# Kernel tuning notes

Measured on AMD Instinct MI355X. Metric: run time of the kernel, lower is better.

Reference implementation:

```python
import jax, jax.numpy as jnp
import numpy as np

H, L, D, R = 16, 4096, 64, 128   # heads, seq len, head dim, FAVOR+ feature dim
S_SCALE = 0.125                  # attention inner-product scaling S
CHUNK = 128                      # chunk size for causal linear attention
EPS = 1e-10                      # module's self.epsilon denominator guard


def _get_proj(d, r, seed=0):
    # get_proj(R, D, orthogonal=True, hyperbolic=True): QR-orthogonalized
    # Gaussian block rescaled by chi column norms, then [W, -W].
    rng = np.random.RandomState(seed)
    rh = r // 2
    w = rng.randn(d, rh)
    chis = np.linalg.norm(w, ord=2, axis=0, keepdims=True)
    qm, _ = np.linalg.qr(w, mode='reduced')
    w = qm * chis
    return np.concatenate((w, -w), axis=1).astype(np.float32)  # (D, R)


def setup_inputs() -> dict:
    key = jax.random.key(0)
    kq, kk, kv = jax.random.split(key, 3)
    q = jax.random.normal(kq, (H, L, D), dtype=jnp.float32)
    k = jax.random.normal(kk, (H, L, D), dtype=jnp.float32)
    v = jax.random.normal(kv, (H, L, D), dtype=jnp.float32)
    W = jnp.asarray(_get_proj(D, R))
    return {"T": 64, "k": k, "q": q, "v": v, "W": W}


def _phi(x, W):
    # FAVOR+ feature map: x' = x * S^0.5 / D^0.25;
    # phi(x) = exp(W^T x' - ||x'||^2 / 2) / sqrt(R)
    xs = x * (S_SCALE ** 0.5 / D ** 0.25)            # (H, L, D)
    Wx = jnp.einsum('hld,dr->hlr', xs, W)            # (H, L, R)
    sq = 0.5 * jnp.sum(xs * xs, axis=-1, keepdims=True)
    return jnp.exp(Wx - sq) / (R ** 0.5)             # (H, L, R)


def reference(T, k, q, v, W):
    # Deterministic FAVOR+ estimator of the strictly-causal softmax attention
    # Pred_l = sum_{j<l} v_j exp(S<q_l,k_j>) / sum_{i<l} exp(S<q_l,k_i>)
    # which the tree+sampling machinery approximates (T = sampling budget,
    # irrelevant for the exact kernel estimate). Chunked linear attention.
    del T
    pq = _phi(q, W)                                  # (H, L, R)
    pk = _phi(k, W)                                  # (H, L, R)
    nc = L // CHUNK
    pq_c = pq.reshape(H, nc, CHUNK, R)
    pk_c = pk.reshape(H, nc, CHUNK, R)
    v_c = v.reshape(H, nc, CHUNK, D)
    # per-chunk KV summaries and exclusive prefix over chunks
    skv = jnp.einsum('hncr,hncd->hnrd', pk_c, v_c)   # (H, nc, R, D)
    zk = jnp.sum(pk_c, axis=2)                       # (H, nc, R)
    skv_prev = jnp.cumsum(skv, axis=1) - skv         # exclusive
    zk_prev = jnp.cumsum(zk, axis=1) - zk
    num_inter = jnp.einsum('hncr,hnrd->hncd', pq_c, skv_prev)
    den_inter = jnp.einsum('hncr,hnr->hnc', pq_c, zk_prev)
    # intra-chunk strictly-causal part (j < l)
    A = jnp.einsum('hncr,hnsr->hncs', pq_c, pk_c)    # (H, nc, C, C)
    mask = jnp.tril(jnp.ones((CHUNK, CHUNK), dtype=A.dtype), k=-1)
    A = A * mask
    num_intra = jnp.einsum('hncs,hnsd->hncd', A, v_c)
    den_intra = jnp.sum(A, axis=-1)
    out = (num_inter + num_intra) / (den_inter + den_intra + EPS)[..., None]
    return out.reshape(H, L, D)
```

## Files before the change

### kernel.cpp

```cpp
#include <hip/hip_runtime.h>
#include <hip/hip_bf16.h>

#define H 16
#define L 4096
#define D 64
#define R 128
#define C2 64
#define NC2 64
#define HN2 (H * NC2)
#define EPS 1e-10f
#define XS_SCALE 0.125f
#define PHI_SCALE 0.08838834764831845f

typedef __attribute__((ext_vector_type(8))) short bf8;
typedef __attribute__((ext_vector_type(4))) short bf4;
typedef __attribute__((ext_vector_type(16))) float facc16;

static __device__ __forceinline__ unsigned short f2b(float f) {
    union { __hip_bfloat16 h; unsigned short u; } c;
    c.h = __float2bfloat16(f);
    return c.u;
}
static __device__ __forceinline__ float b2f(unsigned short s) {
    return __uint_as_float(((unsigned)s) << 16);
}

__global__ __launch_bounds__(256) void kW(const float* __restrict__ W,
                                          unsigned short* __restrict__ WF) {
    __shared__ float wl[8192];
    for (int i = threadIdx.x; i < 8192; i += 256) wl[i] = W[i];
    __syncthreads();
    for (int i = threadIdx.x; i < 1024; i += 256) {
        int tile = i >> 8, s = (i >> 6) & 3, hi = (i >> 5) & 1, lo = i & 31;
        int r = tile * 32 + lo;
        #pragma unroll
        for (int e = 0; e < 8; ++e)
            WF[i * 8 + e] = f2b(wl[(16 * s + 8 * hi + e) * 128 + r]);
    }
}

__global__ __launch_bounds__(256, 4) void k1(
    const float* __restrict__ q, const float* __restrict__ k,
    const float* __restrict__ v, const unsigned short* __restrict__ WF,
    unsigned short* __restrict__ pqF, unsigned short* __restrict__ pkF,
    unsigned short* __restrict__ vTF, unsigned short* __restrict__ skvTp,
    float* __restrict__ zk)
{
    __shared__ __align__(16) unsigned short A_[8192];
    __shared__ __align__(16) unsigned short C_[8192];
    const int tid = threadIdx.x, hn = blockIdx.x;
    const int lane = tid & 63, wave = tid >> 6, lo = lane & 31, hi = lane >> 5;
    const int rg = wave & 1, ch = wave >> 1;
    const size_t cbase = (size_t)hn * C2 * D;

    bf8 af[4];
    float sqrow[16];
    {
        float ssq = 0.f;
        #pragma unroll
        for (int s = 0; s < 4; ++s) {
            const float* qp = q + cbase + (rg * 32 + lo) * 64 + 16 * s + 8 * hi;
            float4 f0 = *(const float4*)qp;
            float4 f1 = *(const float4*)(qp + 4);
            float x0 = f0.x * XS_SCALE, x1 = f0.y * XS_SCALE, x2 = f0.z * XS_SCALE, x3 = f0.w * XS_SCALE;
            float x4 = f1.x * XS_SCALE, x5 = f1.y * XS_SCALE, x6 = f1.z * XS_SCALE, x7 = f1.w * XS_SCALE;
            ssq += x0*x0 + x1*x1 + x2*x2 + x3*x3 + x4*x4 + x5*x5 + x6*x6 + x7*x7;
            bf8 a;
            a[0]=(short)f2b(x0); a[1]=(short)f2b(x1); a[2]=(short)f2b(x2); a[3]=(short)f2b(x3);
            a[4]=(short)f2b(x4); a[5]=(short)f2b(x5); a[6]=(short)f2b(x6); a[7]=(short)f2b(x7);
            af[s] = a;
        }
        ssq += __shfl_xor(ssq, 32); ssq *= 0.5f;
        #pragma unroll
        for (int r2 = 0; r2 < 16; ++r2)
            sqrow[r2] = __shfl(ssq, (r2 & 3) + 8 * (r2 >> 2) + 4 * hi);
    }
    {
        facc16 acc[2];
        #pragma unroll
        for (int t = 0; t < 2; ++t)
            #pragma unroll
            for (int e = 0; e < 16; ++e) acc[t][e] = 0.f;
        #pragma unroll
        for (int s = 0; s < 4; ++s)
            #pragma unroll
            for (int t = 0; t < 2; ++t) {
                const bf8 b = *(const bf8*)(WF + (((2 * ch + t) * 4 + s) * 64 + hi * 32 + lo) * 8);
                acc[t] = __builtin_amdgcn_mfma_f32_32x32x16_bf16(af[s], b, acc[t], 0, 0, 0);
            }
        #pragma unroll
        for (int t = 0; t < 2; ++t)
            #pragma unroll
            for (int reg = 0; reg < 16; ++reg) {
                int row = rg * 32 + (reg & 3) + 8 * (reg >> 2) + 4 * hi;
                int col = (2 * ch + t) * 32 + lo;
                C_[(unsigned)((row * 128 + col) ^ ((row & 15) << 3))] =
                    f2b(__expf(acc[t][reg] - sqrow[reg]) * PHI_SCALE);
            }
    }
    __syncthreads();

    {
        int g2 = wave & 1, sh = wave >> 1;
        #pragma unroll
        for (int s2 = 0; s2 < 4; ++s2) {
            int s = sh * 4 + s2;
            bf8 t8 = *(const bf8*)&C_[(unsigned)(((g2 * 32 + lo) * 128 + 16 * s + 8 * hi) ^ ((lo & 15) << 3))];
            *(bf8*)(pqF + (size_t)hn * 8192 + (size_t)(((g2 * 8 + s) * 64 + hi * 32 + lo) * 8)) = t8;
        }
    }
    float sqk[16];
    {
        float ssq = 0.f;
        #pragma unroll
        for (int s = 0; s < 4; ++s) {
            const float* kp = k + cbase + (rg * 32 + lo) * 64 + 16 * s + 8 * hi;
            float4 f0 = *(const float4*)kp;
            float4 f1 = *(const float4*)(kp + 4);
            float x0 = f0.x * XS_SCALE, x1 = f0.y * XS_SCALE, x2 = f0.z * XS_SCALE, x3 = f0.w * XS_SCALE;
            float x4 = f1.x * XS_SCALE, x5 = f1.y * XS_SCALE, x6 = f1.z * XS_SCALE, x7 = f1.w * XS_SCALE;
            ssq += x0*x0 + x1*x1 + x2*x2 + x3*x3 + x4*x4 + x5*x5 + x6*x6 + x7*x7;
            bf8 a;
            a[0]=(short)f2b(x0); a[1]=(short)f2b(x1); a[2]=(short)f2b(x2); a[3]=(short)f2b(x3);
            a[4]=(short)f2b(x4); a[5]=(short)f2b(x5); a[6]=(short)f2b(x6); a[7]=(short)f2b(x7);
            af[s] = a;
        }
        ssq += __shfl_xor(ssq, 32); ssq *= 0.5f;
        #pragma unroll
        for (int r2 = 0; r2 < 16; ++r2)
            sqk[r2] = __shfl(ssq, (r2 & 3) + 8 * (r2 >> 2) + 4 * hi);
    }
    facc16 acck[2];
    #pragma unroll
    for (int t = 0; t < 2; ++t)
        #pragma unroll
        for (int e = 0; e < 16; ++e) acck[t][e] = 0.f;
    #pragma unroll
    for (int s = 0; s < 4; ++s)
        #pragma unroll
        for (int t = 0; t < 2; ++t) {
            const bf8 b = *(const bf8*)(WF + (((2 * ch + t) * 4 + s) * 64 + hi * 32 + lo) * 8);
            acck[t] = __builtin_amdgcn_mfma_f32_32x32x16_bf16(af[s], b, acck[t], 0, 0, 0);
        }
    __syncthreads();

    #pragma unroll
    for (int t = 0; t < 2; ++t) {
        int colr = (2 * ch + t) * 32 + lo;
        #pragma unroll
        for (int g = 0; g < 4; ++g) {
            int c0 = rg * 32 + 8 * g + 4 * hi;
            bf4 pk4;
            #pragma unroll
            for (int e = 0; e < 4; ++e) {
                unsigned short bb = f2b(__expf(acck[t][4 * g + e] - sqk[4 * g + e]) * PHI_SCALE);
                pk4[e] = (short)bb;
                C_[(unsigned)(((c0 + e) * 128 + colr) ^ (((c0 + e) & 15) << 3))] = bb;
            }
            *(bf4*)&A_[(unsigned)((colr * 64 + c0) ^ ((colr & 7) << 3))] = pk4;
        }
    }
    __syncthreads();

    {
        int g2 = wave & 1, sh = wave >> 1;
        #pragma unroll
        for (int s2 = 0; s2 < 4; ++s2) {
            int s = sh * 4 + s2;
            bf8 t8 = *(const bf8*)&C_[(unsigned)(((g2 * 32 + lo) * 128 + 16 * s + 8 * hi) ^ ((lo & 15) << 3))];
            *(bf8*)(pkF + (size_t)hn * 8192 + (size_t)(((g2 * 8 + s) * 64 + hi * 32 + lo) * 8)) = t8;
        }
    }
    {
        bf8 onesk;
        #pragma unroll
        for (int e = 0; e < 8; ++e) onesk[e] = (lo == 0) ? (short)0x3F80 : (short)0;
        facc16 az;
        #pragma unroll
        for (int e = 0; e < 16; ++e) az[e] = 0.f;
        #pragma unroll
        for (int s = 0; s < 4; ++s) {
            const bf8 a = *(const bf8*)&A_[(unsigned)(((wave * 32 + lo) * 64 + 16 * s + 8 * hi) ^ ((lo & 7) << 3))];
            az = __builtin_amdgcn_mfma_f32_32x32x16_bf16(a, onesk, az, 0, 0, 0);
        }
        if (lo == 0) {
            #pragma unroll
            for (int reg = 0; reg < 16; ++reg)
                zk[(size_t)hn * 128 + wave * 32 + (reg & 3) + 8 * (reg >> 2) + 4 * hi] = az[reg];
        }
    }
    facc16 tv;
    {
        bf8 aid[2];
        #pragma unroll
        for (int s2 = 0; s2 < 2; ++s2)
            #pragma unroll
            for (int e = 0; e < 8; ++e)
                aid[s2][e] = (e == lo - 16 * s2 - 8 * hi) ? (short)0x3F80 : (short)0;
        #pragma unroll
        for (int e = 0; e < 16; ++e) tv[e] = 0.f;
        #pragma unroll
        for (int s2 = 0; s2 < 2; ++s2) {
            const float* vp = v + cbase + (size_t)(32 * rg + lo) * 64 + 16 * (2 * ch + s2) + 8 * hi;
            float4 f0 = *(const float4*)vp;
            float4 f1 = *(const float4*)(vp + 4);
            bf8 b;
            b[0]=(short)f2b(f0.x); b[1]=(short)f2b(f0.y); b[2]=(short)f2b(f0.z); b[3]=(short)f2b(f0.w);
            b[4]=(short)f2b(f1.x); b[5]=(short)f2b(f1.y); b[6]=(short)f2b(f1.z); b[7]=(short)f2b(f1.w);
            tv = __builtin_amdgcn_mfma_f32_32x32x16_bf16(aid[s2], b, tv, 0, 0, 0);
        }
    }
    __syncthreads();

    #pragma unroll
    for (int reg = 0; reg < 16; ++reg) {
        int d = 32 * ch + (reg & 3) + 8 * (reg >> 2) + 4 * hi;
        int c = 32 * rg + lo;
        C_[(unsigned)((d * 64 + c) ^ ((d & 7) << 3))] = f2b(tv[reg]);
    }
    __syncthreads();

    {
        int g2 = wave & 1, sh = wave >> 1;
        #pragma unroll
        for (int s2 = 0; s2 < 2; ++s2) {
            int s = sh * 2 + s2;
            bf8 t8 = *(const bf8*)&C_[(unsigned)(((g2 * 32 + lo) * 64 + 16 * s + 8 * hi) ^ ((lo & 7) << 3))];
            *(bf8*)(vTF + (size_t)hn * 4096 + (size_t)(((g2 * 4 + s) * 64 + hi * 32 + lo) * 8)) = t8;
        }
    }
    {
        facc16 acs[2];
        #pragma unroll
        for (int t = 0; t < 2; ++t)
            #pragma unroll
            for (int e = 0; e < 16; ++e) acs[t][e] = 0.f;
        #pragma unroll
        for (int s = 0; s < 4; ++s) {
            const bf8 a = *(const bf8*)&C_[(unsigned)(((rg * 32 + lo) * 64 + 16 * s + 8 * hi) ^ ((lo & 7) << 3))];
            #pragma unroll
            for (int t = 0; t < 2; ++t) {
                const bf8 b = *(const bf8*)&A_[(unsigned)((((2 * ch + t) * 32 + lo) * 64 + 16 * s + 8 * hi) ^ ((lo & 7) << 3))];
                acs[t] = __builtin_amdgcn_mfma_f32_32x32x16_bf16(a, b, acs[t], 0, 0, 0);
            }
        }
        unsigned short* sg = skvTp + (size_t)hn * 8192;
        #pragma unroll
        for (int t = 0; t < 2; ++t)
            #pragma unroll
            for (int reg = 0; reg < 16; ++reg) {
                int d = rg * 32 + (reg & 3) + 8 * (reg >> 2) + 4 * hi;
                int r = (2 * ch + t) * 32 + lo;
                sg[d * 128 + r] = f2b(acs[t][reg]);
            }
    }
}

__global__ __launch_bounds__(256) void k2(unsigned short* __restrict__ skvTp,
                                          const float* __restrict__ zk,
                                          unsigned short* __restrict__ zkp)
{
    const int bid = blockIdx.x, tid = threadIdx.x;
    if (bid < 512) {
        int g = bid * 256 + tid;
        int h = g >> 13, dr = g & 8191;
        unsigned short* p = skvTp + (size_t)h * NC2 * 8192 + dr;
        unsigned short vals[NC2];
        #pragma unroll
        for (int n = 0; n < NC2; ++n) vals[n] = p[(size_t)n * 8192];
        float run = 0.f;
        #pragma unroll
        for (int n = 0; n < NC2; ++n) {
            float t = b2f(vals[n]);
            p[(size_t)n * 8192] = f2b(run);
            run += t;
        }
    } else {
        int g2 = (bid - 512) * 256 + tid;
        int h = g2 >> 7, r = g2 & 127;
        const float* pz = zk + (size_t)h * NC2 * 128 + r;
        unsigned short* oz = zkp + (size_t)h * NC2 * 128 + r;
        float vals[NC2];
        #pragma unroll
        for (int n = 0; n < NC2; ++n) vals[n] = pz[n * 128];
        float run = 0.f;
        #pragma unroll
        for (int n = 0; n < NC2; ++n) {
            oz[n * 128] = f2b(run);
            run += vals[n];
        }
    }
}

__global__ __launch_bounds__(256) void k3(
    const unsigned short* __restrict__ pqF, const unsigned short* __restrict__ pkF,
    const unsigned short* __restrict__ vTF, const unsigned short* __restrict__ skvTp,
    const unsigned short* __restrict__ zkp, float* __restrict__ out)
{
    __shared__ __align__(16) unsigned short S_[4096];
    const int tid = threadIdx.x, hn = blockIdx.x;
    const int lane = tid & 63, wave = tid >> 6, lo = lane & 31, hi = lane >> 5;
    const int rg = wave & 1, ch = wave >> 1;

    bf8 qf[8];
    #pragma unroll
    for (int s = 0; s < 8; ++s)
        qf[s] = *(const bf8*)(pqF + (size_t)hn * 8192 + (size_t)(((rg * 8 + s) * 64 + hi * 32 + lo) * 8));
    bf8 onesf, zf[8];
    #pragma unroll
    for (int e = 0; e < 8; ++e) onesf[e] = (lo == 0) ? (short)0x3F80 : (short)0;
    #pragma unroll
    for (int s = 0; s < 8; ++s)
        #pragma unroll
        for (int e = 0; e < 8; ++e) zf[s][e] = 0;
    if (lo == 0) {
        #pragma unroll
        for (int s = 0; s < 8; ++s)
            zf[s] = *(const bf8*)(zkp + (size_t)hn * 128 + 16 * s + 8 * hi);
    }

    facc16 ac1;
    #pragma unroll
    for (int e = 0; e < 16; ++e) ac1[e] = 0.f;
    #pragma unroll
    for (int s = 0; s < 8; ++s) {
        const bf8 b = *(const bf8*)(pkF + (size_t)hn * 8192 + (size_t)(((ch * 8 + s) * 64 + hi * 32 + lo) * 8));
        ac1 = __builtin_amdgcn_mfma_f32_32x32x16_bf16(qf[s], b, ac1, 0, 0, 0);
    }
    #pragma unroll
    for (int reg = 0; reg < 16; ++reg) {
        int row = rg * 32 + (reg & 3) + 8 * (reg >> 2) + 4 * hi;
        int sc = ch * 32 + lo;
        S_[(unsigned)((row * 64 + sc) ^ ((row & 7) << 3))] = f2b(sc < row ? ac1[reg] : 0.f);
    }
    __syncthreads();

    facc16 an, ad;
    #pragma unroll
    for (int e = 0; e < 16; ++e) { an[e] = 0.f; ad[e] = 0.f; }
    #pragma unroll
    for (int s = 0; s < 4; ++s) {
        const bf8 a = *(const bf8*)&S_[(unsigned)(((rg * 32 + lo) * 64 + 16 * s + 8 * hi) ^ ((lo & 7) << 3))];
        const bf8 b = *(const bf8*)(vTF + (size_t)hn * 4096 + (size_t)(((ch * 4 + s) * 64 + hi * 32 + lo) * 8));
        an = __builtin_amdgcn_mfma_f32_32x32x16_bf16(a, b, an, 0, 0, 0);
        ad = __builtin_amdgcn_mfma_f32_32x32x16_bf16(a, onesf, ad, 0, 0, 0);
    }
    #pragma unroll
    for (int s = 0; s < 8; ++s) {
        const bf8 b = *(const bf8*)(skvTp + (size_t)hn * 8192 + (size_t)(ch * 32 + lo) * 128 + 16 * s + 8 * hi);
        an = __builtin_amdgcn_mfma_f32_32x32x16_bf16(qf[s], b, an, 0, 0, 0);
        ad = __builtin_amdgcn_mfma_f32_32x32x16_bf16(qf[s], zf[s], ad, 0, 0, 0);
    }
    float* og = out + (size_t)hn * C2 * D;
    #pragma unroll
    for (int reg = 0; reg < 16; ++reg) {
        int row = rg * 32 + (reg & 3) + 8 * (reg >> 2) + 4 * hi;
        float dv = __shfl(ad[reg], lane & 32);
        og[row * 64 + ch * 32 + lo] = an[reg] / (dv + EPS);
    }
}

extern "C" void kernel_launch(void* const* d_in, const int* in_sizes, int n_in,
                              void* d_out, int out_size, void* d_ws, size_t ws_size,
                              hipStream_t stream) {
    const float* k = (const float*)d_in[1];
    const float* q = (const float*)d_in[2];
    const float* v = (const float*)d_in[3];
    const float* W = (const float*)d_in[4];
    float* out = (float*)d_out;

    unsigned short* pqF   = (unsigned short*)d_ws;
    unsigned short* pkF   = pqF + (size_t)HN2 * 8192;
    unsigned short* vTF   = pkF + (size_t)HN2 * 8192;
    unsigned short* skvTp = vTF + (size_t)HN2 * 4096;
    unsigned short* WF    = skvTp + (size_t)HN2 * 8192;
    unsigned short* zkp   = WF + 8192;
    float* zk             = (float*)(zkp + (size_t)HN2 * 128);

    kW<<<1, 256, 0, stream>>>(W, WF);
    k1<<<HN2, 256, 0, stream>>>(q, k, v, WF, pqF, pkF, vTF, skvTp, zk);
    k2<<<520, 256, 0, stream>>>(skvTp, zk, zkp);
    k3<<<HN2, 256, 0, stream>>>(pqF, pkF, vTF, skvTp, zkp, out);
}
```

Before: 54.48 us.

## Compute phi(q) inside k3 instead of storing it from k1

Moves the q feature-map computation (projection, exp) out of k1 and into k3, where phi(q) is written to shared memory and read directly as MFMA operands. This removes the global write and re-read of the bf16 pqF buffer and shortens k1. In exchange k3 reads fp32 q and WF, uses more LDS (an extra 16 KB), and adds a barrier. k1's LDS layout also changes, with V getting its own buffer, which removes one barrier there.

```diff
diff --git a/kernel.cpp b/kernel.cpp
--- a/kernel.cpp
+++ b/kernel.cpp
@@ -40,22 +40,217 @@
 }
 
 __global__ __launch_bounds__(256, 4) void k1(
-    const float* __restrict__ q, const float* __restrict__ k,
-    const float* __restrict__ v, const unsigned short* __restrict__ WF,
-    unsigned short* __restrict__ pqF, unsigned short* __restrict__ pkF,
-    unsigned short* __restrict__ vTF, unsigned short* __restrict__ skvTp,
-    float* __restrict__ zk)
+    const float* __restrict__ k, const float* __restrict__ v,
+    const unsigned short* __restrict__ WF,
+    unsigned short* __restrict__ pkF, unsigned short* __restrict__ vTF,
+    unsigned short* __restrict__ skvTp, float* __restrict__ zk)
 {
+    __shared__ __align__(16) unsigned short C_[8192];
     __shared__ __align__(16) unsigned short A_[8192];
-    __shared__ __align__(16) unsigned short C_[8192];
+    __shared__ __align__(16) unsigned short V_[4096];
     const int tid = threadIdx.x, hn = blockIdx.x;
     const int lane = tid & 63, wave = tid >> 6, lo = lane & 31, hi = lane >> 5;
     const int rg = wave & 1, ch = wave >> 1;
     const size_t cbase = (size_t)hn * C2 * D;
 
     bf8 af[4];
-    float sqrow[16];
-    {
+    float sqk[16];
+    {
+        float ssq = 0.f;
+        #pragma unroll
+        for (int s = 0; s < 4; ++s) {
+            const float* kp = k + cbase + (rg * 32 + lo) * 64 + 16 * s + 8 * hi;
+            float4 f0 = *(const float4*)kp;
+            float4 f1 = *(const float4*)(kp + 4);
+            float x0 = f0.x * XS_SCALE, x1 = f0.y * XS_SCALE, x2 = f0.z * XS_SCALE, x3 = f0.w * XS_SCALE;
+            float x4 = f1.x * XS_SCALE, x5 = f1.y * XS_SCALE, x6 = f1.z * XS_SCALE, x7 = f1.w * XS_SCALE;
+            ssq += x0*x0 + x1*x1 + x2*x2 + x3*x3 + x4*x4 + x5*x5 + x6*x6 + x7*x7;
+            bf8 a;
+            a[0]=(short)f2b(x0); a[1]=(short)f2b(x1); a[2]=(short)f2b(x2); a[3]=(short)f2b(x3);
+            a[4]=(short)f2b(x4); a[5]=(short)f2b(x5); a[6]=(short)f2b(x6); a[7]=(short)f2b(x7);
+            af[s] = a;
+        }
+        ssq += __shfl_xor(ssq, 32); ssq *= 0.5f;
+        #pragma unroll
+        for (int r2 = 0; r2 < 16; ++r2)
+            sqk[r2] = __shfl(ssq, (r2 & 3) + 8 * (r2 >> 2) + 4 * hi);
+    }
+    {
+        facc16 acck[2];
+        #pragma unroll
+        for (int t = 0; t < 2; ++t)
+            #pragma unroll
+            for (int e = 0; e < 16; ++e) acck[t][e] = 0.f;
+        #pragma unroll
+        for (int s = 0; s < 4; ++s)
+            #pragma unroll
+            for (int t = 0; t < 2; ++t) {
+                const bf8 b = *(const bf8*)(WF + (((2 * ch + t) * 4 + s) * 64 + hi * 32 + lo) * 8);
+                acck[t] = __builtin_amdgcn_mfma_f32_32x32x16_bf16(af[s], b, acck[t], 0, 0, 0);
+            }
+        #pragma unroll
+        for (int t = 0; t < 2; ++t) {
+            int colr = (2 * ch + t) * 32 + lo;
+            #pragma unroll
+            for (int g = 0; g < 4; ++g) {
+                int c0 = rg * 32 + 8 * g + 4 * hi;
+                bf4 pk4;
+                #pragma unroll
+                for (int e = 0; e < 4; ++e) {
+                    unsigned short bb = f2b(__expf(acck[t][4 * g + e] - sqk[4 * g + e]) * PHI_SCALE);
+                    pk4[e] = (short)bb;
+                    C_[(unsigned)(((c0 + e) * 128 + colr) ^ (((c0 + e) & 15) << 3))] = bb;
+                }
+                *(bf4*)&A_[(unsigned)((colr * 64 + c0) ^ ((colr & 7) << 3))] = pk4;
+            }
+        }
+    }
+    __syncthreads();
+
+    {
+        int g2 = wave & 1, sh = wave >> 1;
+        #pragma unroll
+        for (int s2 = 0; s2 < 4; ++s2) {
+            int s = sh * 4 + s2;
+            bf8 t8 = *(const bf8*)&C_[(unsigned)(((g2 * 32 + lo) * 128 + 16 * s + 8 * hi) ^ ((lo & 15) << 3))];
+            *(bf8*)(pkF + (size_t)hn * 8192 + (size_t)(((g2 * 8 + s) * 64 + hi * 32 + lo) * 8)) = t8;
+        }
+    }
+    {
+        bf8 onesk;
+        #pragma unroll
+        for (int e = 0; e < 8; ++e) onesk[e] = (lo == 0) ? (short)0x3F80 : (short)0;
+        facc16 az;
+        #pragma unroll
+        for (int e = 0; e < 16; ++e) az[e] = 0.f;
+        #pragma unroll
+        for (int s = 0; s < 4; ++s) {
+            const bf8 a = *(const bf8*)&A_[(unsigned)(((wave * 32 + lo) * 64 + 16 * s + 8 * hi) ^ ((lo & 7) << 3))];
+            az = __builtin_amdgcn_mfma_f32_32x32x16_bf16(a, onesk, az, 0, 0, 0);
+        }
+        if (lo == 0) {
+            #pragma unroll
+            for (int reg = 0; reg < 16; ++reg)
+                zk[(size_t)hn * 128 + wave * 32 + (reg & 3) + 8 * (reg >> 2) + 4 * hi] = az[reg];
+        }
+    }
+    {
+        bf8 aid[2];
+        #pragma unroll
+        for (int s2 = 0; s2 < 2; ++s2)
+            #pragma unroll
+            for (int e = 0; e < 8; ++e)
+                aid[s2][e] = (e == lo - 16 * s2 - 8 * hi) ? (short)0x3F80 : (short)0;
+        facc16 tv;
+        #pragma unroll
+        for (int e = 0; e < 16; ++e) tv[e] = 0.f;
+        #pragma unroll
+        for (int s2 = 0; s2 < 2; ++s2) {
+            const float* vp = v + cbase + (size_t)(32 * rg + lo) * 64 + 16 * (2 * ch + s2) + 8 * hi;
+            float4 f0 = *(const float4*)vp;
+            float4 f1 = *(const float4*)(vp + 4);
+            bf8 b;
+            b[0]=(short)f2b(f0.x); b[1]=(short)f2b(f0.y); b[2]=(short)f2b(f0.z); b[3]=(short)f2b(f0.w);
+            b[4]=(short)f2b(f1.x); b[5]=(short)f2b(f1.y); b[6]=(short)f2b(f1.z); b[7]=(short)f2b(f1.w);
+            tv = __builtin_amdgcn_mfma_f32_32x32x16_bf16(aid[s2], b, tv, 0, 0, 0);
+        }
+        #pragma unroll
+        for (int reg = 0; reg < 16; ++reg) {
+            int d = 32 * ch + (reg & 3) + 8 * (reg >> 2) + 4 * hi;
+            int c = 32 * rg + lo;
+            V_[(unsigned)((d * 64 + c) ^ ((d & 7) << 3))] = f2b(tv[reg]);
+        }
+    }
+    __syncthreads();
+
+    {
+        int g2 = wave & 1, sh = wave >> 1;
+        #pragma unroll
+        for (int s2 = 0; s2 < 2; ++s2) {
+            int s = sh * 2 + s2;
+            bf8 t8 = *(const bf8*)&V_[(unsigned)(((g2 * 32 + lo) * 64 + 16 * s + 8 * hi) ^ ((lo & 7) << 3))];
+            *(bf8*)(vTF + (size_t)hn * 4096 + (size_t)(((g2 * 4 + s) * 64 + hi * 32 + lo) * 8)) = t8;
+        }
+    }
+    {
+        facc16 acs[2];
+        #pragma unroll
+        for (int t = 0; t < 2; ++t)
+            #pragma unroll
+            for (int e = 0; e < 16; ++e) acs[t][e] = 0.f;
+        #pragma unroll
+        for (int s = 0; s < 4; ++s) {
+            const bf8 a = *(const bf8*)&V_[(unsigned)(((rg * 32 + lo) * 64 + 16 * s + 8 * hi) ^ ((lo & 7) << 3))];
+            #pragma unroll
+            for (int t = 0; t < 2; ++t) {
+                const bf8 b = *(const bf8*)&A_[(unsigned)((((2 * ch + t) * 32 + lo) * 64 + 16 * s + 8 * hi) ^ ((lo & 7) << 3))];
+                acs[t] = __builtin_amdgcn_mfma_f32_32x32x16_bf16(a, b, acs[t], 0, 0, 0);
+            }
+        }
+        unsigned short* sg = skvTp + (size_t)hn * 8192;
+        #pragma unroll
+        for (int t = 0; t < 2; ++t)
+            #pragma unroll
+            for (int reg = 0; reg < 16; ++reg) {
+                int d = rg * 32 + (reg & 3) + 8 * (reg >> 2) + 4 * hi;
+                int r = (2 * ch + t) * 32 + lo;
+                sg[d * 128 + r] = f2b(acs[t][reg]);
+            }
+    }
+}
+
+__global__ __launch_bounds__(256) void k2(unsigned short* __restrict__ skvTp,
+                                          const float* __restrict__ zk,
+                                          unsigned short* __restrict__ zkp)
+{
+    const int bid = blockIdx.x, tid = threadIdx.x;
+    if (bid < 512) {
+        int g = bid * 256 + tid;
+        int h = g >> 13, dr = g & 8191;
+        unsigned short* p = skvTp + (size_t)h * NC2 * 8192 + dr;
+        unsigned short vals[NC2];
+        #pragma unroll
+        for (int n = 0; n < NC2; ++n) vals[n] = p[(size_t)n * 8192];
+        float run = 0.f;
+        #pragma unroll
+        for (int n = 0; n < NC2; ++n) {
+            float t = b2f(vals[n]);
+            p[(size_t)n * 8192] = f2b(run);
+            run += t;
+        }
+    } else {
+        int g2 = (bid - 512) * 256 + tid;
+        int h = g2 >> 7, r = g2 & 127;
+        const float* pz = zk + (size_t)h * NC2 * 128 + r;
+        unsigned short* oz = zkp + (size_t)h * NC2 * 128 + r;
+        float vals[NC2];
+        #pragma unroll
+        for (int n = 0; n < NC2; ++n) vals[n] = pz[n * 128];
+        float run = 0.f;
+        #pragma unroll
+        for (int n = 0; n < NC2; ++n) {
+            oz[n * 128] = f2b(run);
+            run += vals[n];
+        }
+    }
+}
+
+__global__ __launch_bounds__(256) void k3(
+    const float* __restrict__ q, const unsigned short* __restrict__ WF,
+    const unsigned short* __restrict__ pkF, const unsigned short* __restrict__ vTF,
+    const unsigned short* __restrict__ skvTp, const unsigned short* __restrict__ zkp,
+    float* __restrict__ out)
+{
+    __shared__ __align__(16) unsigned short P_[8192];
+    __shared__ __align__(16) unsigned short S_[4096];
+    const int tid = threadIdx.x, hn = blockIdx.x;
+    const int lane = tid & 63, wave = tid >> 6, lo = lane & 31, hi = lane >> 5;
+    const int rg = wave & 1, ch = wave >> 1;
+    const size_t cbase = (size_t)hn * C2 * D;
+
+    {
+        bf8 af[4];
+        float sqrow[16];
         float ssq = 0.f;
         #pragma unroll
         for (int s = 0; s < 4; ++s) {
@@ -74,8 +269,7 @@
         #pragma unroll
         for (int r2 = 0; r2 < 16; ++r2)
             sqrow[r2] = __shfl(ssq, (r2 & 3) + 8 * (r2 >> 2) + 4 * hi);
-    }
-    {
+
         facc16 acc[2];
         #pragma unroll
         for (int t = 0; t < 2; ++t)
@@ -94,218 +288,16 @@
             for (int reg = 0; reg < 16; ++reg) {
                 int row = rg * 32 + (reg & 3) + 8 * (reg >> 2) + 4 * hi;
                 int col = (2 * ch + t) * 32 + lo;
-                C_[(unsigned)((row * 128 + col) ^ ((row & 15) << 3))] =
+                P_[(unsigned)((row * 128 + col) ^ ((row & 15) << 3))] =
                     f2b(__expf(acc[t][reg] - sqrow[reg]) * PHI_SCALE);
             }
     }
     __syncthreads();
 
-    {
-        int g2 = wave & 1, sh = wave >> 1;
-        #pragma unroll
-        for (int s2 = 0; s2 < 4; ++s2) {
-            int s = sh * 4 + s2;
-            bf8 t8 = *(const bf8*)&C_[(unsigned)(((g2 * 32 + lo) * 128 + 16 * s + 8 * hi) ^ ((lo & 15) << 3))];
-            *(bf8*)(pqF + (size_t)hn * 8192 + (size_t)(((g2 * 8 + s) * 64 + hi * 32 + lo) * 8)) = t8;
-        }
-    }
-    float sqk[16];
-    {
-        float ssq = 0.f;
-        #pragma unroll
-        for (int s = 0; s < 4; ++s) {
-            const float* kp = k + cbase + (rg * 32 + lo) * 64 + 16 * s + 8 * hi;
-            float4 f0 = *(const float4*)kp;
-            float4 f1 = *(const float4*)(kp + 4);
-            float x0 = f0.x * XS_SCALE, x1 = f0.y * XS_SCALE, x2 = f0.z * XS_SCALE, x3 = f0.w * XS_SCALE;
-            float x4 = f1.x * XS_SCALE, x5 = f1.y * XS_SCALE, x6 = f1.z * XS_SCALE, x7 = f1.w * XS_SCALE;
-            ssq += x0*x0 + x1*x1 + x2*x2 + x3*x3 + x4*x4 + x5*x5 + x6*x6 + x7*x7;
-            bf8 a;
-            a[0]=(short)f2b(x0); a[1]=(short)f2b(x1); a[2]=(short)f2b(x2); a[3]=(short)f2b(x3);
-            a[4]=(short)f2b(x4); a[5]=(short)f2b(x5); a[6]=(short)f2b(x6); a[7]=(short)f2b(x7);
-            af[s] = a;
-        }
-        ssq += __shfl_xor(ssq, 32); ssq *= 0.5f;
-        #pragma unroll
-        for (int r2 = 0; r2 < 16; ++r2)
-            sqk[r2] = __shfl(ssq, (r2 & 3) + 8 * (r2 >> 2) + 4 * hi);
-    }
-    facc16 acck[2];
-    #pragma unroll
-    for (int t = 0; t < 2; ++t)
-        #pragma unroll
-        for (int e = 0; e < 16; ++e) acck[t][e] = 0.f;
-    #pragma unroll
-    for (int s = 0; s < 4; ++s)
-        #pragma unroll
-        for (int t = 0; t < 2; ++t) {
-            const bf8 b = *(const bf8*)(WF + (((2 * ch + t) * 4 + s) * 64 + hi * 32 + lo) * 8);
-            acck[t] = __builtin_amdgcn_mfma_f32_32x32x16_bf16(af[s], b, acck[t], 0, 0, 0);
-        }
-    __syncthreads();
-
-    #pragma unroll
-    for (int t = 0; t < 2; ++t) {
-        int colr = (2 * ch + t) * 32 + lo;
-        #pragma unroll
-        for (int g = 0; g < 4; ++g) {
-            int c0 = rg * 32 + 8 * g + 4 * hi;
-            bf4 pk4;
-            #pragma unroll
-            for (int e = 0; e < 4; ++e) {
-                unsigned short bb = f2b(__expf(acck[t][4 * g + e] - sqk[4 * g + e]) * PHI_SCALE);
-                pk4[e] = (short)bb;
-                C_[(unsigned)(((c0 + e) * 128 + colr) ^ (((c0 + e) & 15) << 3))] = bb;
-            }
-            *(bf4*)&A_[(unsigned)((colr * 64 + c0) ^ ((colr & 7) << 3))] = pk4;
-        }
-    }
-    __syncthreads();
-
-    {
-        int g2 = wave & 1, sh = wave >> 1;
-        #pragma unroll
-        for (int s2 = 0; s2 < 4; ++s2) {
-            int s = sh * 4 + s2;
-            bf8 t8 = *(const bf8*)&C_[(unsigned)(((g2 * 32 + lo) * 128 + 16 * s + 8 * hi) ^ ((lo & 15) << 3))];
-            *(bf8*)(pkF + (size_t)hn * 8192 + (size_t)(((g2 * 8 + s) * 64 + hi * 32 + lo) * 8)) = t8;
-        }
-    }
-    {
-        bf8 onesk;
-        #pragma unroll
-        for (int e = 0; e < 8; ++e) onesk[e] = (lo == 0) ? (short)0x3F80 : (short)0;
-        facc16 az;
-        #pragma unroll
-        for (int e = 0; e < 16; ++e) az[e] = 0.f;
-        #pragma unroll
-        for (int s = 0; s < 4; ++s) {
-            const bf8 a = *(const bf8*)&A_[(unsigned)(((wave * 32 + lo) * 64 + 16 * s + 8 * hi) ^ ((lo & 7) << 3))];
-            az = __builtin_amdgcn_mfma_f32_32x32x16_bf16(a, onesk, az, 0, 0, 0);
-        }
-        if (lo == 0) {
-            #pragma unroll
-            for (int reg = 0; reg < 16; ++reg)
-                zk[(size_t)hn * 128 + wave * 32 + (reg & 3) + 8 * (reg >> 2) + 4 * hi] = az[reg];
-        }
-    }
-    facc16 tv;
-    {
-        bf8 aid[2];
-        #pragma unroll
-        for (int s2 = 0; s2 < 2; ++s2)
-            #pragma unroll
-            for (int e = 0; e < 8; ++e)
-                aid[s2][e] = (e == lo - 16 * s2 - 8 * hi) ? (short)0x3F80 : (short)0;
-        #pragma unroll
-        for (int e = 0; e < 16; ++e) tv[e] = 0.f;
-        #pragma unroll
-        for (int s2 = 0; s2 < 2; ++s2) {
-            const float* vp = v + cbase + (size_t)(32 * rg + lo) * 64 + 16 * (2 * ch + s2) + 8 * hi;
-            float4 f0 = *(const float4*)vp;
-            float4 f1 = *(const float4*)(vp + 4);
-            bf8 b;
-            b[0]=(short)f2b(f0.x); b[1]=(short)f2b(f0.y); b[2]=(short)f2b(f0.z); b[3]=(short)f2b(f0.w);
-            b[4]=(short)f2b(f1.x); b[5]=(short)f2b(f1.y); b[6]=(short)f2b(f1.z); b[7]=(short)f2b(f1.w);
-            tv = __builtin_amdgcn_mfma_f32_32x32x16_bf16(aid[s2], b, tv, 0, 0, 0);
-        }
-    }
-    __syncthreads();
-
-    #pragma unroll
-    for (int reg = 0; reg < 16; ++reg) {
-        int d = 32 * ch + (reg & 3) + 8 * (reg >> 2) + 4 * hi;
-        int c = 32 * rg + lo;
-        C_[(unsigned)((d * 64 + c) ^ ((d & 7) << 3))] = f2b(tv[reg]);
-    }
-    __syncthreads();
-
-    {
-        int g2 = wave & 1, sh = wave >> 1;
-        #pragma unroll
-        for (int s2 = 0; s2 < 2; ++s2) {
-            int s = sh * 2 + s2;
-            bf8 t8 = *(const bf8*)&C_[(unsigned)(((g2 * 32 + lo) * 64 + 16 * s + 8 * hi) ^ ((lo & 7) << 3))];
-            *(bf8*)(vTF + (size_t)hn * 4096 + (size_t)(((g2 * 4 + s) * 64 + hi * 32 + lo) * 8)) = t8;
-        }
-    }
-    {
-        facc16 acs[2];
-        #pragma unroll
-        for (int t = 0; t < 2; ++t)
-            #pragma unroll
-            for (int e = 0; e < 16; ++e) acs[t][e] = 0.f;
-        #pragma unroll
-        for (int s = 0; s < 4; ++s) {
-            const bf8 a = *(const bf8*)&C_[(unsigned)(((rg * 32 + lo) * 64 + 16 * s + 8 * hi) ^ ((lo & 7) << 3))];
-            #pragma unroll
-            for (int t = 0; t < 2; ++t) {
-                const bf8 b = *(const bf8*)&A_[(unsigned)((((2 * ch + t) * 32 + lo) * 64 + 16 * s + 8 * hi) ^ ((lo & 7) << 3))];
-                acs[t] = __builtin_amdgcn_mfma_f32_32x32x16_bf16(a, b, acs[t], 0, 0, 0);
-            }
-        }
-        unsigned short* sg = skvTp + (size_t)hn * 8192;
-        #pragma unroll
-        for (int t = 0; t < 2; ++t)
-            #pragma unroll
-            for (int reg = 0; reg < 16; ++reg) {
-                int d = rg * 32 + (reg & 3) + 8 * (reg >> 2) + 4 * hi;
-                int r = (2 * ch + t) * 32 + lo;
-                sg[d * 128 + r] = f2b(acs[t][reg]);
-            }
-    }
-}
-
-__global__ __launch_bounds__(256) void k2(unsigned short* __restrict__ skvTp,
-                                          const float* __restrict__ zk,
-                                          unsigned short* __restrict__ zkp)
-{
-    const int bid = blockIdx.x, tid = threadIdx.x;
-    if (bid < 512) {
-        int g = bid * 256 + tid;
-        int h = g >> 13, dr = g & 8191;
-        unsigned short* p = skvTp + (size_t)h * NC2 * 8192 + dr;
-        unsigned short vals[NC2];
-        #pragma unroll
-        for (int n = 0; n < NC2; ++n) vals[n] = p[(size_t)n * 8192];
-        float run = 0.f;
-        #pragma unroll
-        for (int n = 0; n < NC2; ++n) {
-            float t = b2f(vals[n]);
-            p[(size_t)n * 8192] = f2b(run);
-            run += t;
-        }
-    } else {
-        int g2 = (bid - 512) * 256 + tid;
-        int h = g2 >> 7, r = g2 & 127;
-        const float* pz = zk + (size_t)h * NC2 * 128 + r;
-        unsigned short* oz = zkp + (size_t)h * NC2 * 128 + r;
-        float vals[NC2];
-        #pragma unroll
-        for (int n = 0; n < NC2; ++n) vals[n] = pz[n * 128];
-        float run = 0.f;
-        #pragma unroll
-        for (int n = 0; n < NC2; ++n) {
-            oz[n * 128] = f2b(run);
-            run += vals[n];
-        }
-    }
-}
-
-__global__ __launch_bounds__(256) void k3(
-    const unsigned short* __restrict__ pqF, const unsigned short* __restrict__ pkF,
-    const unsigned short* __restrict__ vTF, const unsigned short* __restrict__ skvTp,
-    const unsigned short* __restrict__ zkp, float* __restrict__ out)
-{
-    __shared__ __align__(16) unsigned short S_[4096];
-    const int tid = threadIdx.x, hn = blockIdx.x;
-    const int lane = tid & 63, wave = tid >> 6, lo = lane & 31, hi = lane >> 5;
-    const int rg = wave & 1, ch = wave >> 1;
-
     bf8 qf[8];
     #pragma unroll
     for (int s = 0; s < 8; ++s)
-        qf[s] = *(const bf8*)(pqF + (size_t)hn * 8192 + (size_t)(((rg * 8 + s) * 64 + hi * 32 + lo) * 8));
+        qf[s] = *(const bf8*)&P_[(unsigned)(((rg * 32 + lo) * 128 + 16 * s + 8 * hi) ^ ((lo & 15) << 3))];
     bf8 onesf, zf[8];
     #pragma unroll
     for (int e = 0; e < 8; ++e) onesf[e] = (lo == 0) ? (short)0x3F80 : (short)0;
@@ -369,8 +361,7 @@
     const float* W = (const float*)d_in[4];
     float* out = (float*)d_out;
 
-    unsigned short* pqF   = (unsigned short*)d_ws;
-    unsigned short* pkF   = pqF + (size_t)HN2 * 8192;
+    unsigned short* pkF   = (unsigned short*)d_ws;
     unsigned short* vTF   = pkF + (size_t)HN2 * 8192;
     unsigned short* skvTp = vTF + (size_t)HN2 * 4096;
     unsigned short* WF    = skvTp + (size_t)HN2 * 8192;
@@ -378,7 +369,7 @@
     float* zk             = (float*)(zkp + (size_t)HN2 * 128);
 
     kW<<<1, 256, 0, stream>>>(W, WF);
-    k1<<<HN2, 256, 0, stream>>>(q, k, v, WF, pqF, pkF, vTF, skvTp, zk);
+    k1<<<HN2, 256, 0, stream>>>(k, v, WF, pkF, vTF, skvTp, zk);
     k2<<<520, 256, 0, stream>>>(skvTp, zk, zkp);
-    k3<<<HN2, 256, 0, stream>>>(pqF, pkF, vTF, skvTp, zkp, out);
-}
+    k3<<<HN2, 256, 0, stream>>>(q, WF, pkF, vTF, skvTp, zkp, out);
+}
```

New measurement: 55.66 us. 2.2% more time.
